# Optimization experiments

Measured on AMD Instinct MI355X. Metric: run time of the kernel, lower is better.

Reference implementation:

```python
import jax, jax.numpy as jnp
import numpy as np

N = 50000
E = 800000
IN_DIM = 128
OUT_DIM = 128


def setup_inputs() -> dict:
    key = jax.random.key(0)
    k_x, k_e, k_w, k_b = jax.random.split(key, 4)
    x = jax.random.normal(k_x, (N, IN_DIM), dtype=jnp.float32)
    edge_index = jax.random.randint(k_e, (2, E), 0, N, dtype=jnp.int64)
    # nn.Linear(in_dim, out_dim): W [out, in], b [out], uniform(-1/sqrt(in), 1/sqrt(in))
    bound = 1.0 / np.sqrt(IN_DIM)
    W = jax.random.uniform(k_w, (OUT_DIM, IN_DIM), jnp.float32, -bound, bound)
    b = jax.random.uniform(k_b, (OUT_DIM,), jnp.float32, -bound, bound)
    return {"x": x, "edge_index": edge_index, "W": W, "b": b}


def reference(x, edge_index, W, b):
    row, col = edge_index[0], edge_index[1]
    n = x.shape[0]
    # degree of destination nodes (count of incoming edges per node)
    deg = jax.ops.segment_sum(jnp.ones_like(col, dtype=x.dtype), col, num_segments=n)
    deg_inv = jnp.where(deg > 0, 1.0 / deg, 0.0)  # 1/0 -> 0, as in torch code
    norm = deg_inv[col]  # [E]
    msg = x[row] * norm[:, None]  # [E, in_dim]
    out = jax.ops.segment_sum(msg, col, num_segments=n)  # mean of neighbors
    h = x - out  # high-pass filter
    return jax.nn.relu(h @ W.T + b)
```

## Files before the change

### kernel.cpp

```cpp
#include <hip/hip_runtime.h>
#include <hip/hip_bf16.h>

#define DIM 128
#define NB 512
#define BCAP 2048
#define PART_CH 2048
#define SPLIT 4

typedef __attribute__((ext_vector_type(8))) short bf16x8;
typedef __attribute__((ext_vector_type(4))) float f32x4;

__global__ __launch_bounds__(256) void k_init(const float* __restrict__ x,
                                              unsigned short* __restrict__ xb,
                                              int* __restrict__ gcur, int total4) {
    int i = blockIdx.x * 256 + threadIdx.x;
    if (i < NB) gcur[i] = 0;
    if (i >= total4) return;
    float4 v = ((const float4*)x)[i];
    ushort4 o;
    o.x = __hip_bfloat16_raw(__float2bfloat16(v.x)).x;
    o.y = __hip_bfloat16_raw(__float2bfloat16(v.y)).x;
    o.z = __hip_bfloat16_raw(__float2bfloat16(v.z)).x;
    o.w = __hip_bfloat16_raw(__float2bfloat16(v.w)).x;
    ((ushort4*)xb)[i] = o;
}

__global__ __launch_bounds__(256) void k_part(const int* __restrict__ ei,
                                              int* __restrict__ gcur,
                                              unsigned* __restrict__ ebuf,
                                              int nE, int cpb) {
    __shared__ int lh[NB];
    __shared__ int lbase[NB];
    int t = threadIdx.x;
    int base = blockIdx.x * PART_CH;
    for (int i = t; i < NB; i += 256) lh[i] = 0;
    __syncthreads();
    unsigned pk[8];
    int bk[8], rk[8];
    #pragma unroll
    for (int k = 0; k < 8; ++k) {
        int e = base + k * 256 + t;
        if (e < nE) {
            int row = ei[e];
            int col = ei[nE + e];
            int b = (int)((unsigned)col / (unsigned)cpb);
            bk[k] = b;
            pk[k] = ((unsigned)row << 16) | (unsigned)(col - b * cpb);
            rk[k] = atomicAdd(&lh[b], 1);
        } else bk[k] = -1;
    }
    __syncthreads();
    for (int i = t; i < NB; i += 256) {
        int c = lh[i];
        lbase[i] = c ? atomicAdd(&gcur[i], c) : 0;
    }
    __syncthreads();
    #pragma unroll
    for (int k = 0; k < 8; ++k) {
        if (bk[k] >= 0) {
            int pos = lbase[bk[k]] + rk[k];
            if (pos < BCAP) ebuf[(size_t)bk[k] * BCAP + pos] = pk[k];
        }
    }
}

__global__ __launch_bounds__(256) void k_fuse(const float* __restrict__ x,
                                              const unsigned short* __restrict__ xb,
                                              const unsigned* __restrict__ ebuf,
                                              const int* __restrict__ gcur,
                                              float* __restrict__ h, int nN, int cpb) {
    __shared__ unsigned short rowlist[BCAP];
    __shared__ int chist[128];
    __shared__ int cstart[128];
    __shared__ int part[256];
    int b = blockIdx.x / SPLIT;
    int q = blockIdx.x % SPLIT;
    int t = threadIdx.x;
    int c0 = b * cpb;
    int ncols = min(cpb, nN - c0);
    if (ncols <= 0) return;
    int CQ = (cpb + SPLIT - 1) / SPLIT;
    int mylo = q * CQ;
    int myhi = min(mylo + CQ, ncols);
    if (mylo >= ncols) return;
    int ne = min(gcur[b], BCAP);

    if (t < 128) chist[t] = 0;
    __syncthreads();

    unsigned ed[8];
    int rk[8];
    #pragma unroll
    for (int k = 0; k < 8; ++k) {
        int i = k * 256 + t;
        ed[k] = (i < ne) ? ebuf[(size_t)b * BCAP + i] : 0xFFFFFFFFu;
        if (ed[k] != 0xFFFFFFFFu) rk[k] = atomicAdd(&chist[ed[k] & 0xFFFF], 1);
    }
    __syncthreads();

    int v = (t < 128) ? chist[t] : 0;
    part[t] = v;
    __syncthreads();
    for (int off = 1; off < 128; off <<= 1) {
        int add = (t >= off) ? part[t - off] : 0;
        __syncthreads();
        part[t] += add;
        __syncthreads();
    }
    if (t < 128) cstart[t] = part[t] - v;
    __syncthreads();

    #pragma unroll
    for (int k = 0; k < 8; ++k) {
        if (ed[k] != 0xFFFFFFFFu)
            rowlist[cstart[ed[k] & 0xFFFF] + rk[k]] = (unsigned short)(ed[k] >> 16);
    }
    __syncthreads();

    int l = t & 31;
    const ushort4* xb4 = (const ushort4*)xb;
    #define BF2F(u) __uint_as_float(((unsigned)(u)) << 16)
    #define ACC(vv) { a0 += BF2F(vv.x); a1 += BF2F(vv.y); a2 += BF2F(vv.z); a3 += BF2F(vv.w); }
    for (int cc = mylo + (t >> 5); cc < myhi; cc += 8) {
        int cdeg = chist[cc];
        int sb = cstart[cc];
        float a0 = 0.f, a1 = 0.f, a2 = 0.f, a3 = 0.f;
        int j = 0;
        for (; j + 8 <= cdeg; j += 8) {
            int r0 = rowlist[sb + j],     r1 = rowlist[sb + j + 1];
            int r2 = rowlist[sb + j + 2], r3 = rowlist[sb + j + 3];
            int r4 = rowlist[sb + j + 4], r5 = rowlist[sb + j + 5];
            int r6 = rowlist[sb + j + 6], r7 = rowlist[sb + j + 7];
            ushort4 v0 = xb4[(size_t)r0 * 32 + l];
            ushort4 v1 = xb4[(size_t)r1 * 32 + l];
            ushort4 v2 = xb4[(size_t)r2 * 32 + l];
            ushort4 v3 = xb4[(size_t)r3 * 32 + l];
            ushort4 v4 = xb4[(size_t)r4 * 32 + l];
            ushort4 v5 = xb4[(size_t)r5 * 32 + l];
            ushort4 v6 = xb4[(size_t)r6 * 32 + l];
            ushort4 v7 = xb4[(size_t)r7 * 32 + l];
            ACC(v0) ACC(v1) ACC(v2) ACC(v3) ACC(v4) ACC(v5) ACC(v6) ACC(v7)
        }
        for (; j < cdeg; ++j) {
            ushort4 vv = xb4[(size_t)rowlist[sb + j] * 32 + l];
            ACC(vv)
        }
        float dinv = cdeg > 0 ? 1.0f / (float)cdeg : 0.0f;
        int n = c0 + cc;
        float4 xv = ((const float4*)x)[(size_t)n * 32 + l];
        float4 o;
        o.x = xv.x - dinv * a0;
        o.y = xv.y - dinv * a1;
        o.z = xv.z - dinv * a2;
        o.w = xv.w - dinv * a3;
        ((float4*)h)[(size_t)n * 32 + l] = o;
    }
    #undef ACC
    #undef BF2F
}

__global__ __launch_bounds__(256) void hp_gemm(const float* __restrict__ h,
                                               const float* __restrict__ W,
                                               const float* __restrict__ bias,
                                               float* __restrict__ out, int nN) {
    __shared__ unsigned short Wt[DIM][DIM + 8];
    __shared__ unsigned short hsb[64][DIM + 8];
    __shared__ float bs[DIM];
    int t = threadIdx.x;

    #define B16(f) (__hip_bfloat16_raw(__float2bfloat16(f)).x)
    for (int i = t; i < DIM * DIM / 4; i += 256) {
        float4 v = ((const float4*)W)[i];
        int o = i >> 5, k = (i & 31) * 4;
        Wt[o][k] = B16(v.x); Wt[o][k + 1] = B16(v.y);
        Wt[o][k + 2] = B16(v.z); Wt[o][k + 3] = B16(v.w);
    }
    if (t < DIM) bs[t] = bias[t];

    int n0 = blockIdx.x * 64;
    for (int i = t; i < 64 * DIM / 4; i += 256) {
        int r = i >> 5, k = (i & 31) * 4;
        int n = n0 + r;
        float4 v = make_float4(0.f, 0.f, 0.f, 0.f);
        if (n < nN) v = ((const float4*)h)[(size_t)n * 32 + (i & 31)];
        hsb[r][k] = B16(v.x); hsb[r][k + 1] = B16(v.y);
        hsb[r][k + 2] = B16(v.z); hsb[r][k + 3] = B16(v.w);
    }
    #undef B16
    __syncthreads();

    int wv = t >> 6, l = t & 63;
    int lr = l & 15, lg = l >> 4;
    int row0 = wv * 16;

    bf16x8 afrag[4];
    #pragma unroll
    for (int kt = 0; kt < 4; ++kt)
        afrag[kt] = *(const bf16x8*)&hsb[row0 + lr][kt * 32 + lg * 8];

    #pragma unroll
    for (int ot = 0; ot < 8; ++ot) {
        f32x4 acc = {0.f, 0.f, 0.f, 0.f};
        #pragma unroll
        for (int kt = 0; kt < 4; ++kt) {
            bf16x8 bfrag = *(const bf16x8*)&Wt[ot * 16 + lr][kt * 32 + lg * 8];
            acc = __builtin_amdgcn_mfma_f32_16x16x32_bf16(afrag[kt], bfrag, acc, 0, 0, 0);
        }
        int o = ot * 16 + lr;
        float bv = bs[o];
        #pragma unroll
        for (int j = 0; j < 4; ++j) {
            int n = n0 + row0 + lg * 4 + j;
            if (n < nN) out[(size_t)n * DIM + o] = fmaxf(acc[j] + bv, 0.f);
        }
    }
}

extern "C" void kernel_launch(void* const* d_in, const int* in_sizes, int n_in,
                              void* d_out, int out_size, void* d_ws, size_t ws_size,
                              hipStream_t stream) {
    const float* x = (const float*)d_in[0];
    const int* ei = (const int*)d_in[1];
    const float* W = (const float*)d_in[2];
    const float* b = (const float*)d_in[3];
    float* out = (float*)d_out;

    int nN = in_sizes[0] / DIM;
    int nE = in_sizes[1] / 2;

    int* gcur = (int*)d_ws;
    unsigned* ebuf = (unsigned*)(gcur + NB);
    unsigned short* xb = (unsigned short*)(ebuf + (size_t)NB * BCAP);
    float* h = out;

    int cpb = (nN + NB - 1) / NB;
    int nbuckets = (nN + cpb - 1) / cpb;

    int total4 = nN * DIM / 4;
    k_init<<<(total4 + 255) / 256, 256, 0, stream>>>(x, xb, gcur, total4);

    int pblocks = (nE + PART_CH - 1) / PART_CH;
    k_part<<<pblocks, 256, 0, stream>>>(ei, gcur, ebuf, nE, cpb);

    k_fuse<<<nbuckets * SPLIT, 256, 0, stream>>>(x, xb, ebuf, gcur, h, nN, cpb);

    int gblocks = (nN + 63) / 64;
    hp_gemm<<<gblocks, 256, 0, stream>>>(h, W, b, out, nN);
}
```

Measured before the change: 84.96 us.

## Merge cast and partition kernels; store intermediate h as bf16

The bf16 cast of x and the edge partitioning now run as one launch, with blocks split by blockIdx, and the counter reset moves to a memset. This removes a kernel boundary and lets the cast overlap the partition work. The fused aggregation now writes h as bf16 into workspace instead of fp32 into the output buffer. That halves the intermediate write and read traffic and removes the conversion from the GEMM staging loop. The cost is one extra memset launch, and rounding happens at the same point as before.

```diff
diff --git a/kernel.cpp b/kernel.cpp
--- a/kernel.cpp
+++ b/kernel.cpp
@@ -6,32 +6,37 @@
 #define BCAP 2048
 #define PART_CH 2048
 #define SPLIT 4
+#define CAST_PER 1024
 
 typedef __attribute__((ext_vector_type(8))) short bf16x8;
 typedef __attribute__((ext_vector_type(4))) float f32x4;
 
-__global__ __launch_bounds__(256) void k_init(const float* __restrict__ x,
+__global__ __launch_bounds__(256) void k_prep(const int* __restrict__ ei,
+                                              const float* __restrict__ x,
                                               unsigned short* __restrict__ xb,
-                                              int* __restrict__ gcur, int total4) {
-    int i = blockIdx.x * 256 + threadIdx.x;
-    if (i < NB) gcur[i] = 0;
-    if (i >= total4) return;
-    float4 v = ((const float4*)x)[i];
-    ushort4 o;
-    o.x = __hip_bfloat16_raw(__float2bfloat16(v.x)).x;
-    o.y = __hip_bfloat16_raw(__float2bfloat16(v.y)).x;
-    o.z = __hip_bfloat16_raw(__float2bfloat16(v.z)).x;
-    o.w = __hip_bfloat16_raw(__float2bfloat16(v.w)).x;
-    ((ushort4*)xb)[i] = o;
-}
-
-__global__ __launch_bounds__(256) void k_part(const int* __restrict__ ei,
                                               int* __restrict__ gcur,
                                               unsigned* __restrict__ ebuf,
-                                              int nE, int cpb) {
+                                              int nE, int cpb, int PB, int total4) {
+    int t = threadIdx.x;
+    if ((int)blockIdx.x >= PB) {
+        int base = ((int)blockIdx.x - PB) * CAST_PER;
+        #pragma unroll
+        for (int k = 0; k < CAST_PER / 256; ++k) {
+            int i = base + k * 256 + t;
+            if (i < total4) {
+                float4 v = ((const float4*)x)[i];
+                ushort4 o;
+                o.x = __hip_bfloat16_raw(__float2bfloat16(v.x)).x;
+                o.y = __hip_bfloat16_raw(__float2bfloat16(v.y)).x;
+                o.z = __hip_bfloat16_raw(__float2bfloat16(v.z)).x;
+                o.w = __hip_bfloat16_raw(__float2bfloat16(v.w)).x;
+                ((ushort4*)xb)[i] = o;
+            }
+        }
+        return;
+    }
     __shared__ int lh[NB];
     __shared__ int lbase[NB];
-    int t = threadIdx.x;
     int base = blockIdx.x * PART_CH;
     for (int i = t; i < NB; i += 256) lh[i] = 0;
     __syncthreads();
@@ -68,7 +73,8 @@
                                               const unsigned short* __restrict__ xb,
                                               const unsigned* __restrict__ ebuf,
                                               const int* __restrict__ gcur,
-                                              float* __restrict__ h, int nN, int cpb) {
+                                              unsigned short* __restrict__ hb,
+                                              int nN, int cpb) {
     __shared__ unsigned short rowlist[BCAP];
     __shared__ int chist[128];
     __shared__ int cstart[128];
@@ -148,18 +154,18 @@
         float dinv = cdeg > 0 ? 1.0f / (float)cdeg : 0.0f;
         int n = c0 + cc;
         float4 xv = ((const float4*)x)[(size_t)n * 32 + l];
-        float4 o;
-        o.x = xv.x - dinv * a0;
-        o.y = xv.y - dinv * a1;
-        o.z = xv.z - dinv * a2;
-        o.w = xv.w - dinv * a3;
-        ((float4*)h)[(size_t)n * 32 + l] = o;
+        ushort4 o;
+        o.x = __hip_bfloat16_raw(__float2bfloat16(xv.x - dinv * a0)).x;
+        o.y = __hip_bfloat16_raw(__float2bfloat16(xv.y - dinv * a1)).x;
+        o.z = __hip_bfloat16_raw(__float2bfloat16(xv.z - dinv * a2)).x;
+        o.w = __hip_bfloat16_raw(__float2bfloat16(xv.w - dinv * a3)).x;
+        ((ushort4*)hb)[(size_t)n * 32 + l] = o;
     }
     #undef ACC
     #undef BF2F
 }
 
-__global__ __launch_bounds__(256) void hp_gemm(const float* __restrict__ h,
+__global__ __launch_bounds__(256) void hp_gemm(const unsigned short* __restrict__ hb,
                                                const float* __restrict__ W,
                                                const float* __restrict__ bias,
                                                float* __restrict__ out, int nN) {
@@ -175,18 +181,22 @@
         Wt[o][k] = B16(v.x); Wt[o][k + 1] = B16(v.y);
         Wt[o][k + 2] = B16(v.z); Wt[o][k + 3] = B16(v.w);
     }
+    #undef B16
     if (t < DIM) bs[t] = bias[t];
 
     int n0 = blockIdx.x * 64;
-    for (int i = t; i < 64 * DIM / 4; i += 256) {
-        int r = i >> 5, k = (i & 31) * 4;
+    for (int i = t; i < 64 * DIM / 8; i += 256) {
+        int r = i >> 4, k = (i & 15) * 8;
         int n = n0 + r;
-        float4 v = make_float4(0.f, 0.f, 0.f, 0.f);
-        if (n < nN) v = ((const float4*)h)[(size_t)n * 32 + (i & 31)];
-        hsb[r][k] = B16(v.x); hsb[r][k + 1] = B16(v.y);
-        hsb[r][k + 2] = B16(v.z); hsb[r][k + 3] = B16(v.w);
-    }
-    #undef B16
+        ushort4 z = make_ushort4(0, 0, 0, 0);
+        if (n < nN) {
+            *(ushort4*)&hsb[r][k]     = ((const ushort4*)hb)[(size_t)n * 32 + (k >> 2)];
+            *(ushort4*)&hsb[r][k + 4] = ((const ushort4*)hb)[(size_t)n * 32 + (k >> 2) + 1];
+        } else {
+            *(ushort4*)&hsb[r][k] = z;
+            *(ushort4*)&hsb[r][k + 4] = z;
+        }
+    }
     __syncthreads();
 
     int wv = t >> 6, l = t & 63;
@@ -231,19 +241,20 @@
     int* gcur = (int*)d_ws;
     unsigned* ebuf = (unsigned*)(gcur + NB);
     unsigned short* xb = (unsigned short*)(ebuf + (size_t)NB * BCAP);
-    float* h = out;
+    unsigned short* hb = xb + (size_t)nN * DIM;
 
     int cpb = (nN + NB - 1) / NB;
     int nbuckets = (nN + cpb - 1) / cpb;
 
+    hipMemsetAsync(gcur, 0, NB * sizeof(int), stream);
+
     int total4 = nN * DIM / 4;
-    k_init<<<(total4 + 255) / 256, 256, 0, stream>>>(x, xb, gcur, total4);
-
-    int pblocks = (nE + PART_CH - 1) / PART_CH;
-    k_part<<<pblocks, 256, 0, stream>>>(ei, gcur, ebuf, nE, cpb);
-
-    k_fuse<<<nbuckets * SPLIT, 256, 0, stream>>>(x, xb, ebuf, gcur, h, nN, cpb);
+    int PB = (nE + PART_CH - 1) / PART_CH;
+    int CB = (total4 + CAST_PER - 1) / CAST_PER;
+    k_prep<<<PB + CB, 256, 0, stream>>>(ei, x, xb, gcur, ebuf, nE, cpb, PB, total4);
+
+    k_fuse<<<nbuckets * SPLIT, 256, 0, stream>>>(x, xb, ebuf, gcur, hb, nN, cpb);
 
     int gblocks = (nN + 63) / 64;
-    hp_gemm<<<gblocks, 256, 0, stream>>>(h, W, b, out, nN);
-}
+    hp_gemm<<<gblocks, 256, 0, stream>>>(hb, W, b, out, nN);
+}
```

After: 84.12 us. No clear change (-1.0%).

## Apply linear layer before aggregation and merge GEMM with edge partitioning kernel

Applied to the files above, without the earlier changes.

Uses linearity to compute y = x·Wᵀ first (stored as bf16), then gathers neighbour means of y and applies bias and ReLU in the gather kernel. The GEMM blocks run in the same launch as the edge-partition blocks, with a shared-memory union. The separate bf16 conversion kernel and the fp32 intermediate h write/read are removed, and the counter reset becomes a memset. Rounding y to bf16 before aggregation changes numerics slightly, and the launch count drops from four kernels to a memset plus two.

```diff
diff --git a/kernel.cpp b/kernel.cpp
--- a/kernel.cpp
+++ b/kernel.cpp
@@ -10,30 +10,69 @@
 typedef __attribute__((ext_vector_type(8))) short bf16x8;
 typedef __attribute__((ext_vector_type(4))) float f32x4;
 
-__global__ __launch_bounds__(256) void k_init(const float* __restrict__ x,
-                                              unsigned short* __restrict__ xb,
-                                              int* __restrict__ gcur, int total4) {
-    int i = blockIdx.x * 256 + threadIdx.x;
-    if (i < NB) gcur[i] = 0;
-    if (i >= total4) return;
-    float4 v = ((const float4*)x)[i];
-    ushort4 o;
-    o.x = __hip_bfloat16_raw(__float2bfloat16(v.x)).x;
-    o.y = __hip_bfloat16_raw(__float2bfloat16(v.y)).x;
-    o.z = __hip_bfloat16_raw(__float2bfloat16(v.z)).x;
-    o.w = __hip_bfloat16_raw(__float2bfloat16(v.w)).x;
-    ((ushort4*)xb)[i] = o;
-}
-
-__global__ __launch_bounds__(256) void k_part(const int* __restrict__ ei,
-                                              int* __restrict__ gcur,
-                                              unsigned* __restrict__ ebuf,
-                                              int nE, int cpb) {
-    __shared__ int lh[NB];
-    __shared__ int lbase[NB];
+struct PartS { int lh[NB]; int lbase[NB]; };
+struct GemmS { unsigned short Wt[DIM][DIM + 8]; unsigned short xs[64][DIM + 8]; };
+
+__global__ __launch_bounds__(256) void k_partgemm(const int* __restrict__ ei,
+                                                  const float* __restrict__ x,
+                                                  const float* __restrict__ W,
+                                                  int* __restrict__ gcur,
+                                                  unsigned* __restrict__ ebuf,
+                                                  unsigned short* __restrict__ yb,
+                                                  int nE, int cpb, int PB, int nN) {
+    __shared__ union { PartS p; GemmS g; } sm;
     int t = threadIdx.x;
+
+    if ((int)blockIdx.x >= PB) {
+        int n0 = ((int)blockIdx.x - PB) * 64;
+        #define B16(f) (__hip_bfloat16_raw(__float2bfloat16(f)).x)
+        for (int i = t; i < DIM * DIM / 4; i += 256) {
+            float4 v = ((const float4*)W)[i];
+            int o = i >> 5, k = (i & 31) * 4;
+            sm.g.Wt[o][k] = B16(v.x); sm.g.Wt[o][k + 1] = B16(v.y);
+            sm.g.Wt[o][k + 2] = B16(v.z); sm.g.Wt[o][k + 3] = B16(v.w);
+        }
+        for (int i = t; i < 64 * DIM / 4; i += 256) {
+            int r = i >> 5, k = (i & 31) * 4;
+            int n = n0 + r;
+            float4 v = make_float4(0.f, 0.f, 0.f, 0.f);
+            if (n < nN) v = ((const float4*)x)[(size_t)n * 32 + (i & 31)];
+            sm.g.xs[r][k] = B16(v.x); sm.g.xs[r][k + 1] = B16(v.y);
+            sm.g.xs[r][k + 2] = B16(v.z); sm.g.xs[r][k + 3] = B16(v.w);
+        }
+        #undef B16
+        __syncthreads();
+
+        int wv = t >> 6, l = t & 63;
+        int lr = l & 15, lg = l >> 4;
+        int row0 = wv * 16;
+
+        bf16x8 af[4];
+        #pragma unroll
+        for (int kt = 0; kt < 4; ++kt)
+            af[kt] = *(const bf16x8*)&sm.g.xs[row0 + lr][kt * 32 + lg * 8];
+
+        #pragma unroll
+        for (int ot = 0; ot < 8; ++ot) {
+            f32x4 acc = {0.f, 0.f, 0.f, 0.f};
+            #pragma unroll
+            for (int kt = 0; kt < 4; ++kt) {
+                bf16x8 bf = *(const bf16x8*)&sm.g.Wt[ot * 16 + lr][kt * 32 + lg * 8];
+                acc = __builtin_amdgcn_mfma_f32_16x16x32_bf16(af[kt], bf, acc, 0, 0, 0);
+            }
+            int o = ot * 16 + lr;
+            #pragma unroll
+            for (int j = 0; j < 4; ++j) {
+                int n = n0 + row0 + lg * 4 + j;
+                if (n < nN)
+                    yb[(size_t)n * DIM + o] = __hip_bfloat16_raw(__float2bfloat16(acc[j])).x;
+            }
+        }
+        return;
+    }
+
     int base = blockIdx.x * PART_CH;
-    for (int i = t; i < NB; i += 256) lh[i] = 0;
+    for (int i = t; i < NB; i += 256) sm.p.lh[i] = 0;
     __syncthreads();
     unsigned pk[8];
     int bk[8], rk[8];
@@ -46,29 +85,30 @@
             int b = (int)((unsigned)col / (unsigned)cpb);
             bk[k] = b;
             pk[k] = ((unsigned)row << 16) | (unsigned)(col - b * cpb);
-            rk[k] = atomicAdd(&lh[b], 1);
+            rk[k] = atomicAdd(&sm.p.lh[b], 1);
         } else bk[k] = -1;
     }
     __syncthreads();
     for (int i = t; i < NB; i += 256) {
-        int c = lh[i];
-        lbase[i] = c ? atomicAdd(&gcur[i], c) : 0;
+        int c = sm.p.lh[i];
+        sm.p.lbase[i] = c ? atomicAdd(&gcur[i], c) : 0;
     }
     __syncthreads();
     #pragma unroll
     for (int k = 0; k < 8; ++k) {
         if (bk[k] >= 0) {
-            int pos = lbase[bk[k]] + rk[k];
+            int pos = sm.p.lbase[bk[k]] + rk[k];
             if (pos < BCAP) ebuf[(size_t)bk[k] * BCAP + pos] = pk[k];
         }
     }
 }
 
-__global__ __launch_bounds__(256) void k_fuse(const float* __restrict__ x,
-                                              const unsigned short* __restrict__ xb,
-                                              const unsigned* __restrict__ ebuf,
-                                              const int* __restrict__ gcur,
-                                              float* __restrict__ h, int nN, int cpb) {
+__global__ __launch_bounds__(256) void k_gather(const unsigned short* __restrict__ yb,
+                                                const unsigned* __restrict__ ebuf,
+                                                const int* __restrict__ gcur,
+                                                const float* __restrict__ bias,
+                                                float* __restrict__ out,
+                                                int nN, int cpb) {
     __shared__ unsigned short rowlist[BCAP];
     __shared__ int chist[128];
     __shared__ int cstart[128];
@@ -118,7 +158,8 @@
     __syncthreads();
 
     int l = t & 31;
-    const ushort4* xb4 = (const ushort4*)xb;
+    const ushort4* yb4 = (const ushort4*)yb;
+    float4 bv = ((const float4*)bias)[l];
     #define BF2F(u) __uint_as_float(((unsigned)(u)) << 16)
     #define ACC(vv) { a0 += BF2F(vv.x); a1 += BF2F(vv.y); a2 += BF2F(vv.z); a3 += BF2F(vv.w); }
     for (int cc = mylo + (t >> 5); cc < myhi; cc += 8) {
@@ -131,89 +172,32 @@
             int r2 = rowlist[sb + j + 2], r3 = rowlist[sb + j + 3];
             int r4 = rowlist[sb + j + 4], r5 = rowlist[sb + j + 5];
             int r6 = rowlist[sb + j + 6], r7 = rowlist[sb + j + 7];
-            ushort4 v0 = xb4[(size_t)r0 * 32 + l];
-            ushort4 v1 = xb4[(size_t)r1 * 32 + l];
-            ushort4 v2 = xb4[(size_t)r2 * 32 + l];
-            ushort4 v3 = xb4[(size_t)r3 * 32 + l];
-            ushort4 v4 = xb4[(size_t)r4 * 32 + l];
-            ushort4 v5 = xb4[(size_t)r5 * 32 + l];
-            ushort4 v6 = xb4[(size_t)r6 * 32 + l];
-            ushort4 v7 = xb4[(size_t)r7 * 32 + l];
+            ushort4 v0 = yb4[(size_t)r0 * 32 + l];
+            ushort4 v1 = yb4[(size_t)r1 * 32 + l];
+            ushort4 v2 = yb4[(size_t)r2 * 32 + l];
+            ushort4 v3 = yb4[(size_t)r3 * 32 + l];
+            ushort4 v4 = yb4[(size_t)r4 * 32 + l];
+            ushort4 v5 = yb4[(size_t)r5 * 32 + l];
+            ushort4 v6 = yb4[(size_t)r6 * 32 + l];
+            ushort4 v7 = yb4[(size_t)r7 * 32 + l];
             ACC(v0) ACC(v1) ACC(v2) ACC(v3) ACC(v4) ACC(v5) ACC(v6) ACC(v7)
         }
         for (; j < cdeg; ++j) {
-            ushort4 vv = xb4[(size_t)rowlist[sb + j] * 32 + l];
+            ushort4 vv = yb4[(size_t)rowlist[sb + j] * 32 + l];
             ACC(vv)
         }
         float dinv = cdeg > 0 ? 1.0f / (float)cdeg : 0.0f;
         int n = c0 + cc;
-        float4 xv = ((const float4*)x)[(size_t)n * 32 + l];
+        ushort4 sv = yb4[(size_t)n * 32 + l];
         float4 o;
-        o.x = xv.x - dinv * a0;
-        o.y = xv.y - dinv * a1;
-        o.z = xv.z - dinv * a2;
-        o.w = xv.w - dinv * a3;
-        ((float4*)h)[(size_t)n * 32 + l] = o;
+        o.x = fmaxf(BF2F(sv.x) - dinv * a0 + bv.x, 0.f);
+        o.y = fmaxf(BF2F(sv.y) - dinv * a1 + bv.y, 0.f);
+        o.z = fmaxf(BF2F(sv.z) - dinv * a2 + bv.z, 0.f);
+        o.w = fmaxf(BF2F(sv.w) - dinv * a3 + bv.w, 0.f);
+        ((float4*)out)[(size_t)n * 32 + l] = o;
     }
     #undef ACC
     #undef BF2F
-}
-
-__global__ __launch_bounds__(256) void hp_gemm(const float* __restrict__ h,
-                                               const float* __restrict__ W,
-                                               const float* __restrict__ bias,
-                                               float* __restrict__ out, int nN) {
-    __shared__ unsigned short Wt[DIM][DIM + 8];
-    __shared__ unsigned short hsb[64][DIM + 8];
-    __shared__ float bs[DIM];
-    int t = threadIdx.x;
-
-    #define B16(f) (__hip_bfloat16_raw(__float2bfloat16(f)).x)
-    for (int i = t; i < DIM * DIM / 4; i += 256) {
-        float4 v = ((const float4*)W)[i];
-        int o = i >> 5, k = (i & 31) * 4;
-        Wt[o][k] = B16(v.x); Wt[o][k + 1] = B16(v.y);
-        Wt[o][k + 2] = B16(v.z); Wt[o][k + 3] = B16(v.w);
-    }
-    if (t < DIM) bs[t] = bias[t];
-
-    int n0 = blockIdx.x * 64;
-    for (int i = t; i < 64 * DIM / 4; i += 256) {
-        int r = i >> 5, k = (i & 31) * 4;
-        int n = n0 + r;
-        float4 v = make_float4(0.f, 0.f, 0.f, 0.f);
-        if (n < nN) v = ((const float4*)h)[(size_t)n * 32 + (i & 31)];
-        hsb[r][k] = B16(v.x); hsb[r][k + 1] = B16(v.y);
-        hsb[r][k + 2] = B16(v.z); hsb[r][k + 3] = B16(v.w);
-    }
-    #undef B16
-    __syncthreads();
-
-    int wv = t >> 6, l = t & 63;
-    int lr = l & 15, lg = l >> 4;
-    int row0 = wv * 16;
-
-    bf16x8 afrag[4];
-    #pragma unroll
-    for (int kt = 0; kt < 4; ++kt)
-        afrag[kt] = *(const bf16x8*)&hsb[row0 + lr][kt * 32 + lg * 8];
-
-    #pragma unroll
-    for (int ot = 0; ot < 8; ++ot) {
-        f32x4 acc = {0.f, 0.f, 0.f, 0.f};
-        #pragma unroll
-        for (int kt = 0; kt < 4; ++kt) {
-            bf16x8 bfrag = *(const bf16x8*)&Wt[ot * 16 + lr][kt * 32 + lg * 8];
-            acc = __builtin_amdgcn_mfma_f32_16x16x32_bf16(afrag[kt], bfrag, acc, 0, 0, 0);
-        }
-        int o = ot * 16 + lr;
-        float bv = bs[o];
-        #pragma unroll
-        for (int j = 0; j < 4; ++j) {
-            int n = n0 + row0 + lg * 4 + j;
-            if (n < nN) out[(size_t)n * DIM + o] = fmaxf(acc[j] + bv, 0.f);
-        }
-    }
 }
 
 extern "C" void kernel_launch(void* const* d_in, const int* in_sizes, int n_in,
@@ -230,20 +214,16 @@
 
     int* gcur = (int*)d_ws;
     unsigned* ebuf = (unsigned*)(gcur + NB);
-    unsigned short* xb = (unsigned short*)(ebuf + (size_t)NB * BCAP);
-    float* h = out;
+    unsigned short* yb = (unsigned short*)(ebuf + (size_t)NB * BCAP);
 
     int cpb = (nN + NB - 1) / NB;
     int nbuckets = (nN + cpb - 1) / cpb;
 
-    int total4 = nN * DIM / 4;
-    k_init<<<(total4 + 255) / 256, 256, 0, stream>>>(x, xb, gcur, total4);
-
-    int pblocks = (nE + PART_CH - 1) / PART_CH;
-    k_part<<<pblocks, 256, 0, stream>>>(ei, gcur, ebuf, nE, cpb);
-
-    k_fuse<<<nbuckets * SPLIT, 256, 0, stream>>>(x, xb, ebuf, gcur, h, nN, cpb);
-
-    int gblocks = (nN + 63) / 64;
-    hp_gemm<<<gblocks, 256, 0, stream>>>(h, W, b, out, nN);
+    hipMemsetAsync(gcur, 0, NB * sizeof(int), stream);
+
+    int PB = (nE + PART_CH - 1) / PART_CH;
+    int GB = (nN + 63) / 64;
+    k_partgemm<<<PB + GB, 256, 0, stream>>>(ei, x, W, gcur, ebuf, yb, nE, cpb, PB, nN);
+
+    k_gather<<<nbuckets * SPLIT, 256, 0, stream>>>(yb, ebuf, gcur, b, out, nN, cpb);
 }
```

After: 75.90 us. 10.7% less time.
